# Optimization experiments

Measured on AMD Instinct MI355X. Metric: run time of the kernel, lower is better.

The kernel has to match this reference:

```python
import jax, jax.numpy as jnp
import numpy as np


def setup_inputs() -> dict:
    B, C, D = 8192, 2048, 1024
    key = jax.random.key(0)
    kx, kc = jax.random.split(key)
    x = jax.random.normal(kx, (B, D), dtype=jnp.float32)
    # kaiming_normal_ init for centers: std = sqrt(2 / fan_in) with fan_in = feat_dim
    centers = jax.random.normal(kc, (C, D), dtype=jnp.float32) * jnp.sqrt(2.0 / D)
    sigma = jnp.ones((C, D), dtype=jnp.float32)  # nn.init.ones_
    return {"x": x, "centers": centers, "sigma": sigma}


def reference(x, centers, sigma):
    # Original loop computes, per class i:
    #   dist[:, i] = diag(m @ diag(sigma[i]) @ m.T)  with m = x - centers[i]
    # which equals sum_d sigma[i,d] * (x[b,d] - centers[i,d])^2.
    # Expand the square to avoid the O(B*C*D) broadcast intermediate:
    #   dist[b,i] = (x^2) @ sigma[i] - 2 * x @ (sigma[i]*centers[i]) + sum_d sigma[i,d]*centers[i,d]^2
    xsq_term = jnp.einsum('bd,id->bi', x * x, sigma)            # [B, C]
    cross = jnp.einsum('bd,id->bi', x, sigma * centers)          # [B, C]
    const = jnp.sum(sigma * centers * centers, axis=-1)          # [C]
    dist = xsq_term - 2.0 * cross + const[None, :]
    return (centers, sigma, -dist)
```

## Files before the change

### kernel.cpp

```cpp
#include <hip/hip_runtime.h>
#include <hip/hip_bf16.h>


#define B_SZ 8192
#define C_SZ 2048
#define D_SZ 1024
#define K2   2048

typedef __attribute__((ext_vector_type(4))) float f32x4;
typedef __attribute__((ext_vector_type(2))) long lx2;

static __device__ __forceinline__ unsigned int pk4(float a, float b, float c, float d) {
  int v = __builtin_amdgcn_cvt_pk_fp8_f32(a, b, 0, false);
  v = __builtin_amdgcn_cvt_pk_fp8_f32(c, d, v, true);
  return (unsigned int)v;
}

__global__ __launch_bounds__(256) void prep(const float* __restrict__ x,
                                            const float* __restrict__ centers,
                                            const float* __restrict__ sigma,
                                            unsigned char* __restrict__ Aop,
                                            float* __restrict__ out_centers,
                                            float* __restrict__ out_sigma,
                                            unsigned char* __restrict__ Wop,
                                            float* __restrict__ cn) {
  if (blockIdx.x < 4096) {
    const long t = (long)blockIdx.x * 256 + threadIdx.x;
    const long e = t * 8;
    const long b = e >> 10;
    const int  d = (int)(e & 1023);
    const float4* xv = (const float4*)x;
    float4 v0 = xv[2 * t], v1 = xv[2 * t + 1];
    float vs[8] = {v0.x, v0.y, v0.z, v0.w, v1.x, v1.y, v1.z, v1.w};
    uint2 sq, rw;
    sq.x = pk4(vs[0]*vs[0], vs[1]*vs[1], vs[2]*vs[2], vs[3]*vs[3]);
    sq.y = pk4(vs[4]*vs[4], vs[5]*vs[5], vs[6]*vs[6], vs[7]*vs[7]);
    rw.x = pk4(vs[0], vs[1], vs[2], vs[3]);
    rw.y = pk4(vs[4], vs[5], vs[6], vs[7]);
    const int m = (d >> 3) & 7;
    const int destc = (d & ~63) + (m < 4 ? m * 16 : (m - 4) * 16 + 8);
    *(uint2*)(Aop + b * K2 + destc)        = sq;
    *(uint2*)(Aop + b * K2 + 1024 + destc) = rw;
  } else {
    const int grp = threadIdx.x >> 7;
    const int i = (blockIdx.x - 4096) * 2 + grp;
    const int t = threadIdx.x & 127;
    const long base = (long)i * D_SZ;
    const float4* cv = (const float4*)(centers + base);
    const float4* sv = (const float4*)(sigma + base);
    float4 c0 = cv[2 * t], c1 = cv[2 * t + 1];
    float4 s0 = sv[2 * t], s1 = sv[2 * t + 1];
    ((float4*)(out_centers + base))[2 * t]     = c0;
    ((float4*)(out_centers + base))[2 * t + 1] = c1;
    ((float4*)(out_sigma + base))[2 * t]       = s0;
    ((float4*)(out_sigma + base))[2 * t + 1]   = s1;
    float cs[8] = {c0.x, c0.y, c0.z, c0.w, c1.x, c1.y, c1.z, c1.w};
    float ss[8] = {s0.x, s0.y, s0.z, s0.w, s1.x, s1.y, s1.z, s1.w};
    float p = 0.0f;
#pragma unroll
    for (int j = 0; j < 8; ++j) p += ss[j] * cs[j] * cs[j];
    uint2 w1, w2;
    w1.x = pk4(-ss[0], -ss[1], -ss[2], -ss[3]);
    w1.y = pk4(-ss[4], -ss[5], -ss[6], -ss[7]);
    w2.x = pk4(2.f*ss[0]*cs[0], 2.f*ss[1]*cs[1], 2.f*ss[2]*cs[2], 2.f*ss[3]*cs[3]);
    w2.y = pk4(2.f*ss[4]*cs[4], 2.f*ss[5]*cs[5], 2.f*ss[6]*cs[6], 2.f*ss[7]*cs[7]);
    const int m = t & 7;
    const int destc = (t >> 3) * 64 + (m < 4 ? m * 16 : (m - 4) * 16 + 8);
    *(uint2*)(Wop + (long)i * K2 + destc)        = w1;
    *(uint2*)(Wop + (long)i * K2 + 1024 + destc) = w2;
#pragma unroll
    for (int off = 32; off > 0; off >>= 1) p += __shfl_down(p, off, 64);
    __shared__ float red[2][2];
    if ((t & 63) == 0) red[grp][t >> 6] = p;
    __syncthreads();
    if (t == 0) cn[i] = -(red[grp][0] + red[grp][1]);
  }
}

#define VM2()  asm volatile("s_waitcnt vmcnt(2)" ::: "memory")
#define VM0()  asm volatile("s_waitcnt vmcnt(0)" ::: "memory")
#define NOW()  ((void)0)
#define SB()   __builtin_amdgcn_sched_barrier(0)
#define BAR()  __builtin_amdgcn_s_barrier()

#define STAGE_A(C, KT)                                                          \
  do {                                                                          \
    __builtin_amdgcn_global_load_lds(                                           \
        (__attribute__((address_space(1))) void*)(aS + (long)(KT) * 64),        \
        (__attribute__((address_space(3))) void*)(&As[C][tid * 16]), 16, 0, 0); \
    __builtin_amdgcn_global_load_lds(                                           \
        (__attribute__((address_space(1))) void*)(aS + 128 * (long)K2 + (long)(KT) * 64), \
        (__attribute__((address_space(3))) void*)(&As[C][8192 + tid * 16]), 16, 0, 0);    \
  } while (0)

#define STAGE_B(C, KT)                                                          \
  do {                                                                          \
    __builtin_amdgcn_global_load_lds(                                           \
        (__attribute__((address_space(1))) void*)(bS + (long)(KT) * 64),        \
        (__attribute__((address_space(3))) void*)(&Bs[C][tid * 16]), 16, 0, 0); \
    __builtin_amdgcn_global_load_lds(                                           \
        (__attribute__((address_space(1))) void*)(bS + 128 * (long)K2 + (long)(KT) * 64), \
        (__attribute__((address_space(3))) void*)(&Bs[C][8192 + tid * 16]), 16, 0, 0);    \
  } while (0)

#define MMK(AF, BF, SEL)                                                        \
  _Pragma("unroll") for (int mi_ = 0; mi_ < 8; ++mi_)                           \
    _Pragma("unroll") for (int ni_ = 0; ni_ < 4; ++ni_)                         \
      acc[mi_][ni_] = __builtin_amdgcn_mfma_f32_16x16x32_fp8_fp8(               \
          AF[mi_].SEL, BF[ni_].SEL, acc[mi_][ni_], 0, 0, 0);

#define TILE(CA, CB, NA, NB, NBUF, SBUF, U, DOA, DOB, W0, W1, PRE)              \
  {                                                                    \
    if (DOA) STAGE_A(SBUF, (U) + 2);                                            \
    if (PRE) {                                                                  \
      _Pragma("unroll") for (int i_ = 0; i_ < 8; ++i_)                          \
        NA[i_] = *(const lx2*)(&As[NBUF][aBase + i_ * 1024]);                   \
    }                                                                           \
    MMK(CA, CB, x)                                                              \
    SB(); W0(); SB(); BAR();                                                    \
  }                                                                             \
  {                                                                    \
    if (DOB) STAGE_B(SBUF, (U) + 2);                                            \
    if (PRE) {                                                                  \
      _Pragma("unroll") for (int i_ = 0; i_ < 4; ++i_)                          \
        NB[i_] = *(const lx2*)(&Bs[NBUF][bBase + i_ * 1024]);                   \
    }                                                                           \
    MMK(CA, CB, y)                                                              \
    SB(); W1(); SB(); BAR();                                                    \
  }

__global__ __launch_bounds__(512, 2) void gemm256(const unsigned char* __restrict__ A,
                                                  const unsigned char* __restrict__ W,
                                                  const float* __restrict__ cn,
                                                  float* __restrict__ out) {
  __shared__ __attribute__((aligned(16))) unsigned char As[3][16384];
  __shared__ __attribute__((aligned(16))) unsigned char Bs[3][16384];

  const int tid  = threadIdx.x;
  const int lane = tid & 63;
  const int wave = tid >> 6;
  const int wr = wave >> 2;
  const int wc = wave & 3;

  const int bid = blockIdx.x;
  const int xcd = bid & 7, idx = bid >> 3;
  const long rowBase = (long)(xcd * 4 + (idx >> 3)) * 256;
  const long colBase = (long)(idx & 7) * 256;

  const unsigned char* aS = A + (rowBase + (tid >> 2)) * (long)K2 + (tid & 3) * 16;
  const unsigned char* bS = W + (colBase + (tid >> 2)) * (long)K2 + (tid & 3) * 16;

  const int l15 = lane & 15, q = lane >> 4;
  const int aBase = (wr * 128 + l15) * 64 + q * 16;
  const int bBase = (wc * 64 + l15) * 64 + q * 16;

  f32x4 acc[8][4];
#pragma unroll
  for (int i = 0; i < 8; ++i)
#pragma unroll
    for (int j = 0; j < 4; ++j) acc[i][j] = (f32x4){0.f, 0.f, 0.f, 0.f};

  lx2 aA[8], aB[8], bA[4], bB[4];

  STAGE_A(0, 0);
  STAGE_B(0, 0);
  STAGE_A(1, 1);
  STAGE_B(1, 1);
  VM2(); SB(); BAR();
#pragma unroll
  for (int i = 0; i < 8; ++i) aA[i] = *(const lx2*)(&As[0][aBase + i * 1024]);
#pragma unroll
  for (int i = 0; i < 4; ++i) bA[i] = *(const lx2*)(&Bs[0][bBase + i * 1024]);

#pragma unroll 1
  for (int u = 0; u < 30; u += 6) {
    TILE(aA, bA, aB, bB, 1, 2, u + 0, 1, 1, VM2, VM2, 1);
    TILE(aB, bB, aA, bA, 2, 0, u + 1, 1, 1, VM2, VM2, 1);
    TILE(aA, bA, aB, bB, 0, 1, u + 2, 1, 1, VM2, VM2, 1);
    TILE(aB, bB, aA, bA, 1, 2, u + 3, 1, 1, VM2, VM2, 1);
    TILE(aA, bA, aB, bB, 2, 0, u + 4, 1, 1, VM2, VM2, 1);
    TILE(aB, bB, aA, bA, 0, 1, u + 5, 1, 1, VM2, VM2, 1);
  }
  TILE(aA, bA, aB, bB, 1, 2, 30, 0, 0, VM0, NOW, 1);
  TILE(aB, bB, aA, bA, 2, 0, 31, 0, 0, NOW, NOW, 0);

  const int crow = (lane >> 4) * 4;
  const int ccol = lane & 15;
#pragma unroll
  for (int ni = 0; ni < 4; ++ni) {
    const long col = colBase + wc * 64 + ni * 16 + ccol;
    const float c = cn[col];
#pragma unroll
    for (int mi = 0; mi < 8; ++mi) {
      const long row = rowBase + wr * 128 + mi * 16 + crow;
      float* o = out + row * C_SZ + col;
#pragma unroll
      for (int j = 0; j < 4; ++j) o[(long)j * C_SZ] = acc[mi][ni][j] + c;
    }
  }
}

extern "C" void kernel_launch(void* const* d_in, const int* in_sizes, int n_in,
                              void* d_out, int out_size, void* d_ws, size_t ws_size,
                              hipStream_t stream) {
  const float* x       = (const float*)d_in[0];
  const float* centers = (const float*)d_in[1];
  const float* sigma   = (const float*)d_in[2];
  float* out = (float*)d_out;

  unsigned char* Aop = (unsigned char*)d_ws;
  unsigned char* Wop = Aop + (long)B_SZ * K2;
  float* cnp = (float*)(Wop + (long)C_SZ * K2);

  prep<<<4096 + 1024, 256, 0, stream>>>(x, centers, sigma, Aop,
                                        out, out + (size_t)C_SZ * D_SZ, Wop, cnp);

  float* out2 = out + (size_t)2 * C_SZ * D_SZ;
  gemm256<<<256, 512, 0, stream>>>(Aop, Wop, cnp, out2);
}
```

Measured before the change: 77.03 us.

## Shrink GEMM tile to 128x256, add LDS swizzle, drop register double-buffering

The FP8 GEMM tile shrinks from 256x256 to 128x256 rows. The grid doubles to 512 blocks and launch bounds rise to 4 blocks per CU to raise occupancy and fill all CUs. An XOR swizzle on the LDS k-chunk placement aims to cut bank conflicts on fragment reads. The explicit register prefetch of the next fragments is replaced by loads inside each tile step, and the wait count becomes vmcnt(3) to match three loads per stage. The trade-off is lower arithmetic intensity per block, more global traffic for the B operand, and less overlap of LDS reads with MFMA.

After: 69.68 us (median of 2 runs). 1.11x faster.

```diff
diff --git a/kernel.cpp b/kernel.cpp
--- a/kernel.cpp
+++ b/kernel.cpp
@@ -77,21 +77,16 @@
   }
 }
 
-#define VM2()  asm volatile("s_waitcnt vmcnt(2)" ::: "memory")
+#define VM3()  asm volatile("s_waitcnt vmcnt(3)" ::: "memory")
 #define VM0()  asm volatile("s_waitcnt vmcnt(0)" ::: "memory")
 #define NOW()  ((void)0)
 #define SB()   __builtin_amdgcn_sched_barrier(0)
 #define BAR()  __builtin_amdgcn_s_barrier()
 
 #define STAGE_A(C, KT)                                                          \
-  do {                                                                          \
-    __builtin_amdgcn_global_load_lds(                                           \
-        (__attribute__((address_space(1))) void*)(aS + (long)(KT) * 64),        \
-        (__attribute__((address_space(3))) void*)(&As[C][tid * 16]), 16, 0, 0); \
-    __builtin_amdgcn_global_load_lds(                                           \
-        (__attribute__((address_space(1))) void*)(aS + 128 * (long)K2 + (long)(KT) * 64), \
-        (__attribute__((address_space(3))) void*)(&As[C][8192 + tid * 16]), 16, 0, 0);    \
-  } while (0)
+  __builtin_amdgcn_global_load_lds(                                             \
+      (__attribute__((address_space(1))) void*)(aS + (long)(KT) * 64),          \
+      (__attribute__((address_space(3))) void*)(&As[C][tid * 16]), 16, 0, 0)
 
 #define STAGE_B(C, KT)                                                          \
   do {                                                                          \
@@ -103,37 +98,39 @@
         (__attribute__((address_space(3))) void*)(&Bs[C][8192 + tid * 16]), 16, 0, 0);    \
   } while (0)
 
-#define MMK(AF, BF, SEL)                                                        \
-  _Pragma("unroll") for (int mi_ = 0; mi_ < 8; ++mi_)                           \
-    _Pragma("unroll") for (int ni_ = 0; ni_ < 4; ++ni_)                         \
-      acc[mi_][ni_] = __builtin_amdgcn_mfma_f32_16x16x32_fp8_fp8(               \
-          AF[mi_].SEL, BF[ni_].SEL, acc[mi_][ni_], 0, 0, 0);
-
-#define TILE(CA, CB, NA, NB, NBUF, SBUF, U, DOA, DOB, W0, W1, PRE)              \
-  {                                                                    \
-    if (DOA) STAGE_A(SBUF, (U) + 2);                                            \
-    if (PRE) {                                                                  \
-      _Pragma("unroll") for (int i_ = 0; i_ < 8; ++i_)                          \
-        NA[i_] = *(const lx2*)(&As[NBUF][aBase + i_ * 1024]);                   \
-    }                                                                           \
-    MMK(CA, CB, x)                                                              \
-    SB(); W0(); SB(); BAR();                                                    \
-  }                                                                             \
-  {                                                                    \
-    if (DOB) STAGE_B(SBUF, (U) + 2);                                            \
-    if (PRE) {                                                                  \
-      _Pragma("unroll") for (int i_ = 0; i_ < 4; ++i_)                          \
-        NB[i_] = *(const lx2*)(&Bs[NBUF][bBase + i_ * 1024]);                   \
-    }                                                                           \
-    MMK(CA, CB, y)                                                              \
-    SB(); W1(); SB(); BAR();                                                    \
-  }
-
-__global__ __launch_bounds__(512, 2) void gemm256(const unsigned char* __restrict__ A,
+#define TILE(BUF, SBUF, U, DOST, W)                                            \
+  {                                                                            \
+    if (DOST) { STAGE_A(SBUF, (U) + 2); STAGE_B(SBUF, (U) + 2); }              \
+    lx2 a0 = *(const lx2*)(&As[BUF][aBase +    0]);                            \
+    lx2 a1 = *(const lx2*)(&As[BUF][aBase + 1024]);                            \
+    lx2 a2 = *(const lx2*)(&As[BUF][aBase + 2048]);                            \
+    lx2 a3 = *(const lx2*)(&As[BUF][aBase + 3072]);                            \
+    lx2 b0 = *(const lx2*)(&Bs[BUF][bBase +    0]);                            \
+    lx2 b1 = *(const lx2*)(&Bs[BUF][bBase + 1024]);                            \
+    lx2 b2 = *(const lx2*)(&Bs[BUF][bBase + 2048]);                            \
+    lx2 b3 = *(const lx2*)(&Bs[BUF][bBase + 3072]);                            \
+    _Pragma("unroll") for (int mi_ = 0; mi_ < 4; ++mi_) {                      \
+      lx2 am = (mi_ == 0) ? a0 : (mi_ == 1) ? a1 : (mi_ == 2) ? a2 : a3;       \
+      acc[mi_][0] = __builtin_amdgcn_mfma_f32_16x16x32_fp8_fp8(am.x, b0.x, acc[mi_][0], 0,0,0); \
+      acc[mi_][1] = __builtin_amdgcn_mfma_f32_16x16x32_fp8_fp8(am.x, b1.x, acc[mi_][1], 0,0,0); \
+      acc[mi_][2] = __builtin_amdgcn_mfma_f32_16x16x32_fp8_fp8(am.x, b2.x, acc[mi_][2], 0,0,0); \
+      acc[mi_][3] = __builtin_amdgcn_mfma_f32_16x16x32_fp8_fp8(am.x, b3.x, acc[mi_][3], 0,0,0); \
+    }                                                                          \
+    _Pragma("unroll") for (int mi_ = 0; mi_ < 4; ++mi_) {                      \
+      lx2 am = (mi_ == 0) ? a0 : (mi_ == 1) ? a1 : (mi_ == 2) ? a2 : a3;       \
+      acc[mi_][0] = __builtin_amdgcn_mfma_f32_16x16x32_fp8_fp8(am.y, b0.y, acc[mi_][0], 0,0,0); \
+      acc[mi_][1] = __builtin_amdgcn_mfma_f32_16x16x32_fp8_fp8(am.y, b1.y, acc[mi_][1], 0,0,0); \
+      acc[mi_][2] = __builtin_amdgcn_mfma_f32_16x16x32_fp8_fp8(am.y, b2.y, acc[mi_][2], 0,0,0); \
+      acc[mi_][3] = __builtin_amdgcn_mfma_f32_16x16x32_fp8_fp8(am.y, b3.y, acc[mi_][3], 0,0,0); \
+    }                                                                          \
+    SB(); W(); SB(); BAR();                                                    \
+  }
+
+__global__ __launch_bounds__(512, 4) void gemm256(const unsigned char* __restrict__ A,
                                                   const unsigned char* __restrict__ W,
                                                   const float* __restrict__ cn,
                                                   float* __restrict__ out) {
-  __shared__ __attribute__((aligned(16))) unsigned char As[3][16384];
+  __shared__ __attribute__((aligned(16))) unsigned char As[3][8192];
   __shared__ __attribute__((aligned(16))) unsigned char Bs[3][16384];
 
   const int tid  = threadIdx.x;
@@ -144,45 +141,36 @@
 
   const int bid = blockIdx.x;
   const int xcd = bid & 7, idx = bid >> 3;
-  const long rowBase = (long)(xcd * 4 + (idx >> 3)) * 256;
+  const long rowBase = (long)(xcd * 8 + (idx >> 3)) * 128;
   const long colBase = (long)(idx & 7) * 256;
 
-  const unsigned char* aS = A + (rowBase + (tid >> 2)) * (long)K2 + (tid & 3) * 16;
-  const unsigned char* bS = W + (colBase + (tid >> 2)) * (long)K2 + (tid & 3) * 16;
+  const int sl = (tid & 3) ^ ((tid >> 3) & 3);
+  const unsigned char* aS = A + (rowBase + (tid >> 2)) * (long)K2 + sl * 16;
+  const unsigned char* bS = W + (colBase + (tid >> 2)) * (long)K2 + sl * 16;
 
   const int l15 = lane & 15, q = lane >> 4;
-  const int aBase = (wr * 128 + l15) * 64 + q * 16;
-  const int bBase = (wc * 64 + l15) * 64 + q * 16;
-
-  f32x4 acc[8][4];
-#pragma unroll
-  for (int i = 0; i < 8; ++i)
+  const int ck = (q ^ ((l15 >> 1) & 3)) * 16;
+  const int aBase = (wr * 64 + l15) * 64 + ck;
+  const int bBase = (wc * 64 + l15) * 64 + ck;
+
+  f32x4 acc[4][4];
+#pragma unroll
+  for (int i = 0; i < 4; ++i)
 #pragma unroll
     for (int j = 0; j < 4; ++j) acc[i][j] = (f32x4){0.f, 0.f, 0.f, 0.f};
 
-  lx2 aA[8], aB[8], bA[4], bB[4];
-
-  STAGE_A(0, 0);
-  STAGE_B(0, 0);
-  STAGE_A(1, 1);
-  STAGE_B(1, 1);
-  VM2(); SB(); BAR();
-#pragma unroll
-  for (int i = 0; i < 8; ++i) aA[i] = *(const lx2*)(&As[0][aBase + i * 1024]);
-#pragma unroll
-  for (int i = 0; i < 4; ++i) bA[i] = *(const lx2*)(&Bs[0][bBase + i * 1024]);
+  STAGE_A(0, 0); STAGE_B(0, 0);
+  STAGE_A(1, 1); STAGE_B(1, 1);
+  VM3(); SB(); BAR();
 
 #pragma unroll 1
-  for (int u = 0; u < 30; u += 6) {
-    TILE(aA, bA, aB, bB, 1, 2, u + 0, 1, 1, VM2, VM2, 1);
-    TILE(aB, bB, aA, bA, 2, 0, u + 1, 1, 1, VM2, VM2, 1);
-    TILE(aA, bA, aB, bB, 0, 1, u + 2, 1, 1, VM2, VM2, 1);
-    TILE(aB, bB, aA, bA, 1, 2, u + 3, 1, 1, VM2, VM2, 1);
-    TILE(aA, bA, aB, bB, 2, 0, u + 4, 1, 1, VM2, VM2, 1);
-    TILE(aB, bB, aA, bA, 0, 1, u + 5, 1, 1, VM2, VM2, 1);
-  }
-  TILE(aA, bA, aB, bB, 1, 2, 30, 0, 0, VM0, NOW, 1);
-  TILE(aB, bB, aA, bA, 2, 0, 31, 0, 0, NOW, NOW, 0);
+  for (int u = 0; u < 30; u += 3) {
+    TILE(0, 2, u + 0, 1, VM3);
+    TILE(1, 0, u + 1, 1, VM3);
+    TILE(2, 1, u + 2, 1, VM3);
+  }
+  TILE(0, 0, 30, 0, VM0);
+  TILE(1, 0, 31, 0, NOW);
 
   const int crow = (lane >> 4) * 4;
   const int ccol = lane & 15;
@@ -191,8 +179,8 @@
     const long col = colBase + wc * 64 + ni * 16 + ccol;
     const float c = cn[col];
 #pragma unroll
-    for (int mi = 0; mi < 8; ++mi) {
-      const long row = rowBase + wr * 128 + mi * 16 + crow;
+    for (int mi = 0; mi < 4; ++mi) {
+      const long row = rowBase + wr * 64 + mi * 16 + crow;
       float* o = out + row * C_SZ + col;
 #pragma unroll
       for (int j = 0; j < 4; ++j) o[(long)j * C_SZ] = acc[mi][ni][j] + c;
@@ -216,5 +204,5 @@
                                         out, out + (size_t)C_SZ * D_SZ, Wop, cnp);
 
   float* out2 = out + (size_t)2 * C_SZ * D_SZ;
-  gemm256<<<256, 512, 0, stream>>>(Aop, Wop, cnp, out2);
-}
+  gemm256<<<512, 512, 0, stream>>>(Aop, Wop, cnp, out2);
+}
```
